# Kernel optimization log

Measured on AMD Instinct MI355X. Metric: run time of the kernel, lower is better.

## Reference

```python
import jax, jax.numpy as jnp
import numpy as np

DIM_K = 128
MODEL_DIM = 1024
B, S = 8, 2048

def setup_inputs() -> dict:
    key = jax.random.key(0)
    k1, k2, k3, k4, k5, k6, k7 = jax.random.split(key, 7)
    return {
        "query": jax.random.normal(k1, (B, S, MODEL_DIM), dtype=jnp.float32),
        "key": jax.random.normal(k2, (B, S, MODEL_DIM), dtype=jnp.float32),
        "value": jax.random.normal(k3, (B, S, MODEL_DIM), dtype=jnp.float32),
        "mask": jax.random.randint(k4, (B, S, S), 0, 2, dtype=jnp.int32),
        # nn.Linear(model_dim, dim_k, bias=False): weight shape [dim_k, model_dim]
        "Wq": jax.random.normal(k5, (DIM_K, MODEL_DIM), dtype=jnp.float32) * (MODEL_DIM ** -0.5),
        "Wk": jax.random.normal(k6, (DIM_K, MODEL_DIM), dtype=jnp.float32) * (MODEL_DIM ** -0.5),
        "Wv": jax.random.normal(k7, (DIM_K, MODEL_DIM), dtype=jnp.float32) * (MODEL_DIM ** -0.5),
    }

def reference(query, key, value, mask, Wq, Wk, Wv):
    # projections: y = x @ W.T
    q = jnp.einsum('bsm,km->bsk', query, Wq)
    k = jnp.einsum('bsm,km->bsk', key, Wk)
    v = jnp.einsum('bsm,km->bsk', value, Wv)
    scale = 1.0 / jnp.sqrt(jnp.float32(DIM_K))
    pre_score = jnp.einsum('bqk,bsk->bqs', q, k) * scale  # [B,Sq,Sk]
    pre_score = jnp.where(mask == 0, jnp.float32(-1e9), pre_score)
    score = jax.nn.softmax(pre_score, axis=-1)
    return jnp.einsum('bqs,bsk->bqk', score, v)
```

## Files before the change

kernel.cpp:

```cpp
#include <hip/hip_runtime.h>
#include <hip/hip_fp16.h>

#define SEQ 2048
#define DMODEL 1024
#define DK 128

typedef _Float16 f16x8 __attribute__((ext_vector_type(8)));
typedef float    f32x4 __attribute__((ext_vector_type(4)));

#define L2E 1.44269504088896340736f

#define WS_Q  393216
#define WS_K  2490368
#define WS_VT 4587520
#define WS_F16_BYTES 13369344ull

__global__ __launch_bounds__(256) void wconv_kernel(
    const float* __restrict__ wq, const float* __restrict__ wk,
    const float* __restrict__ wv, _Float16* __restrict__ w16)
{
    int i = blockIdx.x * 256 + threadIdx.x;
    int p = i >> 17;
    int j = i & 131071;
    const float* src = (p == 0) ? wq : ((p == 1) ? wk : wv);
    float f = src[j];
    if (p == 0) f *= 0.08838834764831845f;
    w16[i] = (_Float16)f;
}

__global__ __launch_bounds__(256) void proj_kernel(
    const float* __restrict__ xq, const float* __restrict__ xk,
    const float* __restrict__ xv, const _Float16* __restrict__ w16,
    _Float16* __restrict__ qws, _Float16* __restrict__ kws, _Float16* __restrict__ vtws)
{
    const int p = blockIdx.y;
    const float* __restrict__ x = (p == 0) ? xq : ((p == 1) ? xk : xv);
    const _Float16* __restrict__ w = w16 + p * 131072;

    const int mtile = blockIdx.x;
    const int m0 = mtile << 6;
    const int t = threadIdx.x;
    const int wv_ = t >> 6;
    const int lane = t & 63;
    const int l15 = lane & 15, g = lane >> 4;
    const int mw = m0 + wv_ * 16;

    f32x4 acc[8];
#pragma unroll
    for (int nt = 0; nt < 8; ++nt) acc[nt] = (f32x4){0.f, 0.f, 0.f, 0.f};

    const float* x0 = x + (size_t)(mw + l15) * 1024 + g * 8;
    const _Float16* wb = w + (size_t)l15 * 1024 + g * 8;

    f32x4 a0 = *(const f32x4*)(x0);
    f32x4 a1 = *(const f32x4*)(x0 + 4);
    f16x8 bA[8], bB[8];
#pragma unroll
    for (int nt = 0; nt < 8; ++nt)
        bA[nt] = *(const f16x8*)(wb + (size_t)nt * 16384);

    for (int ks = 0; ks < 32; ks += 2) {
        f32x4 a2 = *(const f32x4*)(x0 + ks * 32 + 32);
        f32x4 a3 = *(const f32x4*)(x0 + ks * 32 + 36);
#pragma unroll
        for (int nt = 0; nt < 8; ++nt)
            bB[nt] = *(const f16x8*)(wb + (size_t)nt * 16384 + ks * 32 + 32);
        f16x8 af;
#pragma unroll
        for (int j = 0; j < 4; ++j) { af[j] = (_Float16)a0[j]; af[4 + j] = (_Float16)a1[j]; }
#pragma unroll
        for (int nt = 0; nt < 8; ++nt)
            acc[nt] = __builtin_amdgcn_mfma_f32_16x16x32_f16(af, bA[nt], acc[nt], 0, 0, 0);

        if (ks + 2 < 32) {
            a0 = *(const f32x4*)(x0 + ks * 32 + 64);
            a1 = *(const f32x4*)(x0 + ks * 32 + 68);
#pragma unroll
            for (int nt = 0; nt < 8; ++nt)
                bA[nt] = *(const f16x8*)(wb + (size_t)nt * 16384 + ks * 32 + 64);
        }
        f16x8 ag;
#pragma unroll
        for (int j = 0; j < 4; ++j) { ag[j] = (_Float16)a2[j]; ag[4 + j] = (_Float16)a3[j]; }
#pragma unroll
        for (int nt = 0; nt < 8; ++nt)
            acc[nt] = __builtin_amdgcn_mfma_f32_16x16x32_f16(ag, bB[nt], acc[nt], 0, 0, 0);
    }

    __shared__ __align__(16) _Float16 olds[9216];
#pragma unroll
    for (int nt = 0; nt < 8; ++nt)
#pragma unroll
        for (int r = 0; r < 4; ++r) {
            int rowl = wv_ * 16 + g * 4 + r;
            int col = nt * 16 + l15;
            _Float16 v = (_Float16)acc[nt][r];
            if (p < 2) olds[rowl * 136 + col] = v;
            else       olds[col * 72 + rowl] = v;
        }
    __syncthreads();

    if (p < 2) {
#pragma unroll
        for (int i = 0; i < 4; ++i) {
            int idx = i * 256 + t;
            int row = idx >> 4, ck = idx & 15;
            f16x8 v = *(const f16x8*)(olds + row * 136 + ck * 8);
            _Float16* dst = ((p == 0) ? qws : kws) + (size_t)(m0 + row) * 128 + ck * 8;
            *(f16x8*)dst = v;
        }
    } else {
        const int bq = mtile >> 5, s0 = (mtile & 31) << 6;
#pragma unroll
        for (int i = 0; i < 4; ++i) {
            int idx = i * 256 + t;
            int row = idx >> 3, ck = idx & 7;
            f16x8 v = *(const f16x8*)(olds + row * 72 + ck * 8);
            _Float16* dst = vtws + ((size_t)(bq * 128 + row)) * 2048 + s0 + ck * 8;
            *(f16x8*)dst = v;
        }
    }
}

__global__ __launch_bounds__(256) void flash_kernel(
    const _Float16* __restrict__ qws, const _Float16* __restrict__ kws,
    const _Float16* __restrict__ vtws, const int* __restrict__ mask,
    float* __restrict__ out, float* __restrict__ part, float* __restrict__ mlbuf,
    int ktp)
{
    const int bb = blockIdx.x & 7;
    const int rest = blockIdx.x >> 3;
    const int mtile = rest & 31;
    const int jsplit = rest >> 5;
    const int sq0 = mtile << 6;
    const int t = threadIdx.x;
    const int wv_ = t >> 6;
    const int lane = t & 63;
    const int l15 = lane & 15, g = lane >> 4;

    __shared__ __align__(16) _Float16 smem[22528];
    _Float16* klds = smem;
    _Float16* vtlds = smem + 8704;
    _Float16* plds = smem + 17920 + wv_ * 1152;

    f16x8 qf[4];
    {
        const _Float16* qp = qws + ((size_t)(bb * 2048 + sq0 + wv_ * 16 + l15)) * 128 + g * 8;
#pragma unroll
        for (int ks = 0; ks < 4; ++ks) qf[ks] = *(const f16x8*)(qp + ks * 32);
    }

    f32x4 o[8];
#pragma unroll
    for (int nt = 0; nt < 8; ++nt) o[nt] = (f32x4){0.f, 0.f, 0.f, 0.f};
    float m_run[4], l_run[4];
#pragma unroll
    for (int r = 0; r < 4; ++r) { m_run[r] = -__builtin_inff(); l_run[r] = 0.f; }

    const int* mbase = mask + ((size_t)(bb * 2048 + sq0 + wv_ * 16 + g * 4)) * 2048 + l15;

    const int kt_begin = jsplit * ktp, kt_end = kt_begin + ktp;
    for (int kt = kt_begin; kt < kt_end; ++kt) {
        const int n0 = kt << 6;
        __syncthreads();
#pragma unroll
        for (int i = 0; i < 8; ++i) {
            int idx = i * 256 + t;
            if (idx < 1024) {
                int row = idx >> 4, ck = idx & 15;
                *(f16x8*)(klds + row * 136 + ck * 8) =
                    *(const f16x8*)(kws + ((size_t)(bb * 2048 + n0 + row)) * 128 + ck * 8);
            } else {
                int v = idx - 1024;
                int row = v >> 3, ck = v & 7;
                *(f16x8*)(vtlds + row * 72 + ck * 8) =
                    *(const f16x8*)(vtws + ((size_t)(bb * 128 + row)) * 2048 + n0 + ck * 8);
            }
        }
        __syncthreads();

        int mv[4][4];
#pragma unroll
        for (int nt = 0; nt < 4; ++nt)
#pragma unroll
            for (int r = 0; r < 4; ++r)
                mv[nt][r] = mbase[(size_t)r * 2048 + n0 + nt * 16];

        f32x4 sf[4];
#pragma unroll
        for (int nt = 0; nt < 4; ++nt) sf[nt] = (f32x4){0.f, 0.f, 0.f, 0.f};
#pragma unroll
        for (int nt = 0; nt < 4; ++nt) {
            const _Float16* kp = klds + (nt * 16 + l15) * 136 + g * 8;
#pragma unroll
            for (int ks = 0; ks < 4; ++ks) {
                f16x8 bfk = *(const f16x8*)(kp + ks * 32);
                sf[nt] = __builtin_amdgcn_mfma_f32_16x16x32_f16(qf[ks], bfk, sf[nt], 0, 0, 0);
            }
        }

        float mx[4], mnew[4], alpha[4], psum[4];
#pragma unroll
        for (int r = 0; r < 4; ++r)
            mx[r] = fmaxf(fmaxf(sf[0][r], sf[1][r]), fmaxf(sf[2][r], sf[3][r]));
#pragma unroll
        for (int off = 1; off < 16; off <<= 1)
#pragma unroll
            for (int r = 0; r < 4; ++r)
                mx[r] = fmaxf(mx[r], __shfl_xor(mx[r], off, 64));
#pragma unroll
        for (int r = 0; r < 4; ++r) {
            mnew[r] = fmaxf(m_run[r], mx[r]);
            alpha[r] = exp2f((m_run[r] - mnew[r]) * L2E);
            psum[r] = 0.f;
        }
#pragma unroll
        for (int nt = 0; nt < 4; ++nt)
#pragma unroll
            for (int r = 0; r < 4; ++r) {
                float pv = exp2f((sf[nt][r] - mnew[r]) * L2E);
                pv = mv[nt][r] ? pv : 0.f;
                psum[r] += pv;
                plds[(g * 4 + r) * 72 + nt * 16 + l15] = (_Float16)pv;
            }
#pragma unroll
        for (int off = 1; off < 16; off <<= 1)
#pragma unroll
            for (int r = 0; r < 4; ++r)
                psum[r] += __shfl_xor(psum[r], off, 64);
#pragma unroll
        for (int r = 0; r < 4; ++r) {
            l_run[r] = l_run[r] * alpha[r] + psum[r];
            m_run[r] = mnew[r];
        }
#pragma unroll
        for (int nt = 0; nt < 8; ++nt)
#pragma unroll
            for (int r = 0; r < 4; ++r) o[nt][r] *= alpha[r];

        f16x8 pa[2];
#pragma unroll
        for (int ks2 = 0; ks2 < 2; ++ks2)
            pa[ks2] = *(const f16x8*)(plds + l15 * 72 + ks2 * 32 + g * 8);

#pragma unroll
        for (int nt2 = 0; nt2 < 8; ++nt2) {
            const _Float16* vp = vtlds + (nt2 * 16 + l15) * 72 + g * 8;
#pragma unroll
            for (int ks2 = 0; ks2 < 2; ++ks2) {
                f16x8 bfv = *(const f16x8*)(vp + ks2 * 32);
                o[nt2] = __builtin_amdgcn_mfma_f32_16x16x32_f16(pa[ks2], bfv, o[nt2], 0, 0, 0);
            }
        }
    }

    if (part == nullptr) {
        float inv[4];
#pragma unroll
        for (int r = 0; r < 4; ++r) inv[r] = 1.0f / l_run[r];
#pragma unroll
        for (int nt2 = 0; nt2 < 8; ++nt2)
#pragma unroll
            for (int r = 0; r < 4; ++r)
                out[((size_t)(bb * 2048 + sq0 + wv_ * 16 + g * 4 + r)) * 128 + nt2 * 16 + l15] =
                    o[nt2][r] * inv[r];
    } else {
#pragma unroll
        for (int nt2 = 0; nt2 < 8; ++nt2)
#pragma unroll
            for (int r = 0; r < 4; ++r) {
                size_t rowg = (size_t)(bb * 2048 + sq0 + wv_ * 16 + g * 4 + r);
                part[((size_t)jsplit * 16384 + rowg) * 128 + nt2 * 16 + l15] = o[nt2][r];
            }
        if (l15 == 0) {
#pragma unroll
            for (int r = 0; r < 4; ++r) {
                size_t rowg = (size_t)(bb * 2048 + sq0 + wv_ * 16 + g * 4 + r);
                mlbuf[((size_t)jsplit * 16384 + rowg) * 2]     = m_run[r];
                mlbuf[((size_t)jsplit * 16384 + rowg) * 2 + 1] = l_run[r];
            }
        }
    }
}

__global__ __launch_bounds__(256) void merge_kernel(
    const float* __restrict__ part, const float* __restrict__ mlbuf,
    float* __restrict__ out, int J)
{
    int t = threadIdx.x;
    size_t row = (size_t)blockIdx.x * 8 + (t >> 5);
    int c = (t & 31) * 4;
    float mj[4];
    float m = -__builtin_inff();
    for (int j = 0; j < J; ++j) {
        mj[j] = mlbuf[((size_t)j * 16384 + row) * 2];
        m = fmaxf(m, mj[j]);
    }
    float l = 0.f;
    f32x4 acc = (f32x4){0.f, 0.f, 0.f, 0.f};
    for (int j = 0; j < J; ++j) {
        float w = exp2f((mj[j] - m) * L2E);
        l += w * mlbuf[((size_t)j * 16384 + row) * 2 + 1];
        f32x4 v = *(const f32x4*)(part + ((size_t)j * 16384 + row) * 128 + c);
#pragma unroll
        for (int e = 0; e < 4; ++e) acc[e] += w * v[e];
    }
    float inv = 1.0f / l;
#pragma unroll
    for (int e = 0; e < 4; ++e) acc[e] *= inv;
    *(f32x4*)(out + row * 128 + c) = acc;
}

extern "C" void kernel_launch(void* const* d_in, const int* in_sizes, int n_in,
                              void* d_out, int out_size, void* d_ws, size_t ws_size,
                              hipStream_t stream)
{
    const float* query = (const float*)d_in[0];
    const float* key   = (const float*)d_in[1];
    const float* value = (const float*)d_in[2];
    const int*   mask  = (const int*)d_in[3];
    const float* Wq    = (const float*)d_in[4];
    const float* Wk    = (const float*)d_in[5];
    const float* Wv    = (const float*)d_in[6];
    float* out = (float*)d_out;

    _Float16* w16 = (_Float16*)d_ws;
    _Float16* qws = w16 + WS_Q;
    _Float16* kws = w16 + WS_K;
    _Float16* vtws = w16 + WS_VT;

    const size_t per_split = 16384ull * 128 * 4 + 16384ull * 8;
    int J = 1;
    if (ws_size >= WS_F16_BYTES + 4 * per_split)      J = 4;
    else if (ws_size >= WS_F16_BYTES + 2 * per_split) J = 2;
    float* part = (J > 1) ? (float*)((char*)d_ws + WS_F16_BYTES) : nullptr;
    float* mlbuf = (J > 1) ? (part + (size_t)J * 16384 * 128) : nullptr;

    wconv_kernel<<<1536, 256, 0, stream>>>(Wq, Wk, Wv, w16);
    proj_kernel<<<dim3(256, 3), 256, 0, stream>>>(query, key, value, w16, qws, kws, vtws);
    flash_kernel<<<256 * J, 256, 0, stream>>>(qws, kws, vtws, mask, out, part, mlbuf, 32 / J);
    if (J > 1) merge_kernel<<<2048, 256, 0, stream>>>(part, mlbuf, out, J);
}
```

Measured before the change: 449.6 us.

## Stage projection weight tiles through double-buffered LDS instead of per-wave global loads

The projection kernel previously had each of the four waves load the full 128-column fp16 weight slice straight from global memory, so every weight element was fetched four times per block. It now loads each 128x64 weight tile once per block with a cooperative load, writes it to a padded, double-buffered shared-memory tile, and has all waves read their MFMA operands from LDS. Global loads for the next tile are issued before the MFMAs run, and launch bounds request three blocks per CU. In exchange the kernel uses more LDS, adds a barrier per k-step, and the occupancy hint may force register spilling.

```diff
diff --git a/kernel.cpp b/kernel.cpp
--- a/kernel.cpp
+++ b/kernel.cpp
@@ -28,7 +28,7 @@
     w16[i] = (_Float16)f;
 }
 
-__global__ __launch_bounds__(256) void proj_kernel(
+__global__ __launch_bounds__(256, 3) void proj_kernel(
     const float* __restrict__ xq, const float* __restrict__ xk,
     const float* __restrict__ xv, const _Float16* __restrict__ w16,
     _Float16* __restrict__ qws, _Float16* __restrict__ kws, _Float16* __restrict__ vtws)
@@ -45,49 +45,69 @@
     const int l15 = lane & 15, g = lane >> 4;
     const int mw = m0 + wv_ * 16;
 
+    __shared__ __align__(16) _Float16 smem[18432];
+
     f32x4 acc[8];
 #pragma unroll
     for (int nt = 0; nt < 8; ++nt) acc[nt] = (f32x4){0.f, 0.f, 0.f, 0.f};
 
     const float* x0 = x + (size_t)(mw + l15) * 1024 + g * 8;
-    const _Float16* wb = w + (size_t)l15 * 1024 + g * 8;
-
-    f32x4 a0 = *(const f32x4*)(x0);
-    f32x4 a1 = *(const f32x4*)(x0 + 4);
-    f16x8 bA[8], bB[8];
-#pragma unroll
-    for (int nt = 0; nt < 8; ++nt)
-        bA[nt] = *(const f16x8*)(wb + (size_t)nt * 16384);
-
-    for (int ks = 0; ks < 32; ks += 2) {
-        f32x4 a2 = *(const f32x4*)(x0 + ks * 32 + 32);
-        f32x4 a3 = *(const f32x4*)(x0 + ks * 32 + 36);
-#pragma unroll
-        for (int nt = 0; nt < 8; ++nt)
-            bB[nt] = *(const f16x8*)(wb + (size_t)nt * 16384 + ks * 32 + 32);
-        f16x8 af;
-#pragma unroll
-        for (int j = 0; j < 4; ++j) { af[j] = (_Float16)a0[j]; af[4 + j] = (_Float16)a1[j]; }
-#pragma unroll
-        for (int nt = 0; nt < 8; ++nt)
-            acc[nt] = __builtin_amdgcn_mfma_f32_16x16x32_f16(af, bA[nt], acc[nt], 0, 0, 0);
-
-        if (ks + 2 < 32) {
-            a0 = *(const f32x4*)(x0 + ks * 32 + 64);
-            a1 = *(const f32x4*)(x0 + ks * 32 + 68);
-#pragma unroll
-            for (int nt = 0; nt < 8; ++nt)
-                bA[nt] = *(const f16x8*)(wb + (size_t)nt * 16384 + ks * 32 + 64);
-        }
-        f16x8 ag;
-#pragma unroll
-        for (int j = 0; j < 4; ++j) { ag[j] = (_Float16)a2[j]; ag[4 + j] = (_Float16)a3[j]; }
-#pragma unroll
-        for (int nt = 0; nt < 8; ++nt)
-            acc[nt] = __builtin_amdgcn_mfma_f32_16x16x32_f16(ag, bB[nt], acc[nt], 0, 0, 0);
-    }
-
-    __shared__ __align__(16) _Float16 olds[9216];
+    const int srow = t >> 3, skc = t & 7;
+    const _Float16* wsrc = w + (size_t)srow * 1024 + skc * 8;
+    const int sdst = srow * 72 + skc * 8;
+
+    f16x8 wreg[2][4];
+    f32x4 areg[2][4];
+
+#pragma unroll
+    for (int j = 0; j < 4; ++j)
+        wreg[0][j] = *(const f16x8*)(wsrc + (size_t)j * 32 * 1024);
+#pragma unroll
+    for (int s = 0; s < 2; ++s) {
+        areg[0][s * 2]     = *(const f32x4*)(x0 + s * 32);
+        areg[0][s * 2 + 1] = *(const f32x4*)(x0 + s * 32 + 4);
+    }
+
+#pragma unroll
+    for (int kt = 0; kt < 16; ++kt) {
+        const int c = kt & 1;
+        _Float16* buf = smem + c * 9216;
+
+#pragma unroll
+        for (int j = 0; j < 4; ++j)
+            *(f16x8*)(buf + j * 32 * 72 + sdst) = wreg[c][j];
+        __syncthreads();
+
+        if (kt < 15) {
+#pragma unroll
+            for (int j = 0; j < 4; ++j)
+                wreg[c ^ 1][j] = *(const f16x8*)(wsrc + (size_t)j * 32 * 1024
+                                                 + (kt + 1) * 64);
+#pragma unroll
+            for (int s = 0; s < 2; ++s) {
+                areg[c ^ 1][s * 2]     = *(const f32x4*)(x0 + (kt + 1) * 64 + s * 32);
+                areg[c ^ 1][s * 2 + 1] = *(const f32x4*)(x0 + (kt + 1) * 64 + s * 32 + 4);
+            }
+        }
+
+#pragma unroll
+        for (int s = 0; s < 2; ++s) {
+            f16x8 af;
+#pragma unroll
+            for (int j = 0; j < 4; ++j) {
+                af[j]     = (_Float16)areg[c][s * 2][j];
+                af[4 + j] = (_Float16)areg[c][s * 2 + 1][j];
+            }
+#pragma unroll
+            for (int nt = 0; nt < 8; ++nt) {
+                f16x8 bf = *(const f16x8*)(buf + (nt * 16 + l15) * 72 + s * 32 + g * 8);
+                acc[nt] = __builtin_amdgcn_mfma_f32_16x16x32_f16(af, bf, acc[nt], 0, 0, 0);
+            }
+        }
+    }
+
+    __syncthreads();
+    _Float16* olds = smem;
 #pragma unroll
     for (int nt = 0; nt < 8; ++nt)
 #pragma unroll
```

Result: faster. 381.6 us (-15.1%).
